# Kernel tuning notes

Measured on AMD Instinct MI355X. Metric: run time of the kernel, lower is better.

Reference implementation:

```python
import jax, jax.numpy as jnp
import numpy as np

B = 1024      # molecules in batch
M = 128       # atoms per molecule
K = 32        # max_num_neighbors
CUTOFF = 5.0  # radius cutoff


def setup_inputs() -> dict:
    key = jax.random.key(0)
    pos = jax.random.normal(key, (B * M, 3), dtype=jnp.float32) * 3.0
    batch = (jnp.arange(B * M, dtype=jnp.int32) // M).astype(jnp.int32)
    return {"pos": pos, "batch": batch}


def reference(pos, batch):
    # pos: [N,3]; batch is sorted with M atoms per molecule -> reshape [B,M,3]
    p = pos.reshape(B, M, 3)
    sq = jnp.sum(p * p, axis=-1)  # [B,M]
    # per-molecule pairwise squared distances, [B,M,M]
    d2 = sq[:, :, None] + sq[:, None, :] - 2.0 * jnp.einsum('bic,bjc->bij', p, p)
    d2 = jnp.maximum(d2, 0.0)
    valid = d2 < CUTOFF * CUTOFF  # loop=True: self (d2=0) is included
    d2m = jnp.where(valid, d2, jnp.inf)
    neg, idx = jax.lax.top_k(-d2m, K)       # K nearest in-radius, idx: [B,M,K]
    taken = jnp.isfinite(neg)                # which slots are real edges
    local_i = jnp.arange(M, dtype=idx.dtype)
    idx = jnp.where(taken, idx, local_i[None, :, None])  # pad with self index

    # gather neighbor positions: [B,M,K,3]
    p_nb = p[jnp.arange(B)[:, None, None], idx]
    vec = p_nb - p[:, :, None, :]            # pos[edge0] - pos[edge1] (source - target)

    nonself = idx != local_i[None, :, None]
    mask = taken & nonself                   # self-loops & padding get weight 0
    sqv = jnp.sum(vec * vec, axis=-1)
    weight = jnp.where(mask, jnp.sqrt(jnp.where(mask, sqv, 1.0)), 0.0)

    node_base = (jnp.arange(B, dtype=jnp.int32) * M)[:, None, None]
    src = (node_base + idx.astype(jnp.int32)).reshape(-1)                 # edge_index[0] = neighbor j
    dst = jnp.broadcast_to(node_base + local_i.astype(jnp.int32)[None, :, None], (B, M, K)).reshape(-1)
    edge_index = jnp.stack([src, dst], axis=0)          # [2, B*M*K]
    edge_weight = weight.reshape(-1)                    # [B*M*K]
    edge_vec = vec.reshape(-1, 3)                       # [B*M*K, 3]
    return edge_index, edge_weight, edge_vec
```

## Files before the change

kernel.cpp:

```cpp
#include <hip/hip_runtime.h>
#include <stdint.h>

#define BB 1024
#define MM 128
#define KK 32
#define NEDGE (BB * MM * KK)
#define BPB 4
#define ROWS_PER_WAVE (MM / (4 * BPB))

#define TH 0x41C80000u
#define INFK 0x7F800000u

typedef unsigned int uint2v __attribute__((ext_vector_type(2)));

#define DPP1 "quad_perm:[1,0,3,2] row_mask:0xf bank_mask:0xf"
#define DPP2 "quad_perm:[2,3,0,1] row_mask:0xf bank_mask:0xf"

template<int ST>
static __device__ __forceinline__ void cexd(unsigned& k, unsigned long long msk) {
    unsigned t0, t1;
    if constexpr (ST == 1) {
        asm("s_nop 1\n\t"
            "v_min_u32_dpp %1, %0, %0 " DPP1 "\n\t"
            "v_max_u32_dpp %2, %0, %0 " DPP1 "\n\t"
            "v_cndmask_b32 %0, %2, %1, %3"
            : "+v"(k), "=&v"(t0), "=&v"(t1) : "s"(msk));
    } else {
        asm("s_nop 1\n\t"
            "v_min_u32_dpp %1, %0, %0 " DPP2 "\n\t"
            "v_max_u32_dpp %2, %0, %0 " DPP2 "\n\t"
            "v_cndmask_b32 %0, %2, %1, %3"
            : "+v"(k), "=&v"(t0), "=&v"(t1) : "s"(msk));
    }
}

template<int ST>
static __device__ __forceinline__ void cexs(unsigned& k, unsigned long long msk) {
    unsigned p = (unsigned)__builtin_amdgcn_ds_swizzle((int)k, (ST << 10) | 0x1F);
    unsigned mn = __builtin_elementwise_min(k, p);
    unsigned mx = __builtin_elementwise_max(k, p);
    asm("v_cndmask_b32 %0, %1, %2, %3" : "=v"(k) : "v"(mx), "v"(mn), "s"(msk));
}

static __device__ __forceinline__ void cex32f(unsigned& k, unsigned long long msk) {
#if __has_builtin(__builtin_amdgcn_permlane32_swap)
    uint2v s = __builtin_amdgcn_permlane32_swap(k, k, false, false);
    unsigned mn = __builtin_elementwise_min(s.x, s.y);
    unsigned mx = __builtin_elementwise_max(s.x, s.y);
#else
    unsigned p = (unsigned)__shfl_xor((int)k, 32, 64);
    unsigned mn = __builtin_elementwise_min(k, p);
    unsigned mx = __builtin_elementwise_max(k, p);
#endif
    asm("v_cndmask_b32 %0, %1, %2, %3" : "=v"(k) : "v"(mx), "v"(mn), "s"(msk));
}

static __device__ __forceinline__ unsigned minxor32(unsigned k) {
#if __has_builtin(__builtin_amdgcn_permlane32_swap)
    uint2v s = __builtin_amdgcn_permlane32_swap(k, k, false, false);
    return __builtin_elementwise_min(s.x, s.y);
#else
    unsigned p = (unsigned)__shfl_xor((int)k, 32, 64);
    return __builtin_elementwise_min(k, p);
#endif
}

static __device__ __forceinline__ unsigned mbcnt64(unsigned long long m) {
    unsigned t = __builtin_amdgcn_mbcnt_lo((unsigned)m, 0u);
    return __builtin_amdgcn_mbcnt_hi((unsigned)(m >> 32), t);
}

__global__ __launch_bounds__(256, 4) void knn_edges_kernel(const float* __restrict__ pos,
                                                           float* __restrict__ out) {
    __shared__ float px[MM], py[MM], pz[MM], sqs[MM];
    __shared__ unsigned comp[4][64];
    const int blk = blockIdx.x;
    const int b = blk >> 2;
    const int sub = blk & (BPB - 1);
    const int tid = threadIdx.x;

    if (tid < MM) {
        const float* p = pos + (size_t)(b * MM + tid) * 3;
        float x = p[0], y = p[1], z = p[2];
        px[tid] = x; py[tid] = y; pz[tid] = z;
        sqs[tid] = __fadd_rn(__fadd_rn(__fmul_rn(x, x), __fmul_rn(y, y)), __fmul_rn(z, z));
    }
    __syncthreads();

    const int wave = tid >> 6;
    const int lane = tid & 63;
    const int g = lane & 31;
    const bool hi = lane >= 32;
    const unsigned upper = hi ? ~0u : 0u;

    unsigned long long m1  = 0x5555555555555555ull;
    unsigned long long m2  = 0x3333333333333333ull;
    unsigned long long m4  = 0x0F0F0F0F0F0F0F0Full;
    unsigned long long m8  = 0x00FF00FF00FF00FFull;
    unsigned long long m16 = 0x0000FFFF0000FFFFull;
    unsigned long long m32 = 0x00000000FFFFFFFFull;
    asm("" : "+s"(m1), "+s"(m2), "+s"(m4), "+s"(m8), "+s"(m16), "+s"(m32));

    auto dmask = [&](int s) -> unsigned {
        unsigned zer = ((g & s) == 0) ? ~0u : 0u;
        return ~(zer ^ upper);
    };
    const unsigned f2    = dmask(2);
    const unsigned nf2   = ~f2;
    const unsigned f4c   = dmask(4);
    const unsigned f8c   = dmask(8);
    const unsigned f16c  = dmask(16);
    const unsigned f32c  = dmask(32);
    const unsigned t24   = f2 ^ f4c;
    const unsigned t48   = f4c ^ f8c;
    const unsigned t816  = f8c ^ f16c;
    const unsigned t1632 = f16c ^ f32c;
    const unsigned nf32  = ~f32c;

    auto ff = [&](int s) -> unsigned { return (lane & s) ? ~0u : 0u; };
    const unsigned u2    = ff(2);
    const unsigned s24   = u2 ^ ff(4);
    const unsigned s48   = ff(4) ^ ff(8);
    const unsigned s816  = ff(8) ^ ff(16);
    const unsigned s1632 = ff(16) ^ ff(32);
    const unsigned u32   = ff(32);

    const int j0 = lane, j1 = lane + 64;
    const float xa = px[j0], ya = py[j0], za = pz[j0], qa = sqs[j0];
    const float xb = px[j1], yb = py[j1], zb = pz[j1], qb = sqs[j1];

    const int row0 = sub * (MM / BPB) + wave * ROWS_PER_WAVE;
    const float fbase = (float)(b * MM);

    float* const vecbase = out + 3 * (size_t)NEDGE;
    const long e0 = (long)(b * MM + row0) * KK + g;
    float* pA = hi ? out + (size_t)NEDGE + e0 : out + e0;
    float* pB = vecbase + e0 * 3 + (hi ? 2 : 0);
    float* pC = hi ? out + 2 * (size_t)NEDGE + e0 : vecbase + e0 * 3 + 1;
    const int sC = hi ? KK : 3 * KK;

    float fnode = (float)(b * MM + row0);

    for (int i = row0; i < row0 + ROWS_PER_WAVE; ++i) {
        const float xi = px[i], yi = py[i], zi = pz[i], qi = sqs[i];

        float dot0 = fmaf(xi, xa, fmaf(yi, ya, zi * za));
        float d20 = fmaxf(fmaf(-2.0f, dot0, qi + qa), 0.0f);
        unsigned k0r = (__float_as_uint(d20) & 0xFFFFFF80u) | (unsigned)j0;
        float dot1 = fmaf(xi, xb, fmaf(yi, yb, zi * zb));
        float d21 = fmaxf(fmaf(-2.0f, dot1, qi + qb), 0.0f);
        unsigned k1r = (__float_as_uint(d21) & 0xFFFFFF80u) | (unsigned)j1;

        unsigned long long mask0 = __ballot(k0r < TH);
        unsigned long long mask1 = __ballot(k1r < TH);
        unsigned c0 = (unsigned)__popcll(mask0);
        unsigned nsurv = c0 + (unsigned)__popcll(mask1);

        unsigned mdup;
        if (nsurv <= 64u) {
            unsigned dest0 = mbcnt64(mask0);
            unsigned dest1 = c0 + mbcnt64(mask1);
            if (k0r < TH) comp[wave][dest0] = k0r;
            if (k1r < TH) comp[wave][dest1] = k1r;
            asm volatile("s_waitcnt lgkmcnt(0)" ::: "memory");
            unsigned k = comp[wave][lane];
            k = ((unsigned)lane < nsurv) ? k : INFK;

            k ^= u2;
            cexd<1>(k, m1);
            k ^= s24;
            cexd<2>(k, m2); cexd<1>(k, m1);
            k ^= s48;
            cexs<4>(k, m4); cexd<2>(k, m2); cexd<1>(k, m1);
            k ^= s816;
            cexs<8>(k, m8); cexs<4>(k, m4); cexd<2>(k, m2); cexd<1>(k, m1);
            k ^= s1632;
            cexs<16>(k, m16); cexs<8>(k, m8); cexs<4>(k, m4);
            cexd<2>(k, m2); cexd<1>(k, m1);
            k ^= u32;
            cex32f(k, m32); cexs<16>(k, m16); cexs<8>(k, m8); cexs<4>(k, m4);
            cexd<2>(k, m2); cexd<1>(k, m1);

#if __has_builtin(__builtin_amdgcn_permlane32_swap)
            uint2v s = __builtin_amdgcn_permlane32_swap(k, k, false, false);
            unsigned partner = s.x ^ s.y ^ k;
#else
            unsigned partner = (unsigned)__shfl_xor((int)k, 32, 64);
#endif
            asm("v_cndmask_b32 %0, %1, %2, %3" : "=v"(mdup) : "v"(partner), "v"(k), "s"(m32));
        } else {
            unsigned K0 = k0r ^ f2;
            unsigned K1 = k1r ^ nf2;
#define SS2(ST, MSK) cexs<ST>(K0, MSK); cexs<ST>(K1, MSK);
            SS2(1, m1)
            K0 ^= t24; K1 ^= t24;
            SS2(2, m2) SS2(1, m1)
            K0 ^= t48; K1 ^= t48;
            SS2(4, m4) SS2(2, m2) SS2(1, m1)
            K0 ^= t816; K1 ^= t816;
            SS2(8, m8) SS2(4, m4) SS2(2, m2) SS2(1, m1)
            K0 ^= t1632; K1 ^= t1632;
            SS2(16, m16) SS2(8, m8) SS2(4, m4) SS2(2, m2) SS2(1, m1)
#undef SS2
            unsigned Ca = (__builtin_elementwise_min(K0 ^ f32c, K1 ^ nf32)) ^ upper;
            cexs<16>(Ca, m16); cexs<8>(Ca, m8); cexs<4>(Ca, m4);
            cexs<2>(Ca, m2);  cexs<1>(Ca, m1);
            unsigned Ma = minxor32(Ca ^ upper);
            cexs<16>(Ma, m16); cexs<8>(Ma, m8); cexs<4>(Ma, m4);
            cexs<2>(Ma, m2);  cexs<1>(Ma, m1);
            mdup = Ma;
        }

        const bool taken = mdup < TH;
        const int j = (int)(mdup & 127u);
        const int sel = taken ? j : i;

        float dxv = __fsub_rn(px[sel], xi);
        float dyv = __fsub_rn(py[sel], yi);
        float dzv = __fsub_rn(pz[sel], zi);
        float w = sqrtf(fmaf(dzv, dzv, fmaf(dyv, dyv, dxv * dxv)));
        const float fsrc = fbase + (float)sel;

        pA[0] = hi ? fnode : fsrc;
        pB[0] = hi ? dzv : dxv;
        pC[0] = hi ? w : dyv;
        pA += KK; pB += 3 * KK; pC += sC;
        fnode += 1.0f;
    }
}

extern "C" void kernel_launch(void* const* d_in, const int* in_sizes, int n_in,
                              void* d_out, int out_size, void* d_ws, size_t ws_size,
                              hipStream_t stream) {
    const float* pos = (const float*)d_in[0];
    float* out = (float*)d_out;
    hipLaunchKernelGGL(knn_edges_kernel, dim3(BB * BPB), dim3(256), 0, stream, pos, out);
}
```

Before: 39.68 us.

## Add tighter second radius filter and process one molecule per block

When more than 64 atoms fall inside the cutoff, the kernel retries compaction with a smaller threshold (d2 < 12.5). If that leaves between 32 and 64 candidates, it uses the cheap single-register bitonic sort instead of the full 128-element sort. It also drops the four-blocks-per-molecule split: one block now handles a whole molecule with 32 rows per wave, which cuts redundant position loads but reduces grid parallelism to 1024 blocks. The extra ballot adds a little cost on dense rows.

```diff
diff --git a/kernel.cpp b/kernel.cpp
--- a/kernel.cpp
+++ b/kernel.cpp
@@ -5,10 +5,10 @@
 #define MM 128
 #define KK 32
 #define NEDGE (BB * MM * KK)
-#define BPB 4
-#define ROWS_PER_WAVE (MM / (4 * BPB))
-
-#define TH 0x41C80000u
+#define ROWS_PER_WAVE 32
+
+#define TH  0x41C80000u
+#define T2  0x41480000u
 #define INFK 0x7F800000u
 
 typedef unsigned int uint2v __attribute__((ext_vector_type(2)));
@@ -65,6 +65,18 @@
 #endif
 }
 
+static __device__ __forceinline__ unsigned duphalf(unsigned k, unsigned long long m32) {
+#if __has_builtin(__builtin_amdgcn_permlane32_swap)
+    uint2v s = __builtin_amdgcn_permlane32_swap(k, k, false, false);
+    unsigned partner = s.x ^ s.y ^ k;
+#else
+    unsigned partner = (unsigned)__shfl_xor((int)k, 32, 64);
+#endif
+    unsigned r;
+    asm("v_cndmask_b32 %0, %1, %2, %3" : "=v"(r) : "v"(partner), "v"(k), "s"(m32));
+    return r;
+}
+
 static __device__ __forceinline__ unsigned mbcnt64(unsigned long long m) {
     unsigned t = __builtin_amdgcn_mbcnt_lo((unsigned)m, 0u);
     return __builtin_amdgcn_mbcnt_hi((unsigned)(m >> 32), t);
@@ -74,9 +86,7 @@
                                                            float* __restrict__ out) {
     __shared__ float px[MM], py[MM], pz[MM], sqs[MM];
     __shared__ unsigned comp[4][64];
-    const int blk = blockIdx.x;
-    const int b = blk >> 2;
-    const int sub = blk & (BPB - 1);
+    const int b = blockIdx.x;
     const int tid = threadIdx.x;
 
     if (tid < MM) {
@@ -100,6 +110,14 @@
     unsigned long long m16 = 0x0000FFFF0000FFFFull;
     unsigned long long m32 = 0x00000000FFFFFFFFull;
     asm("" : "+s"(m1), "+s"(m2), "+s"(m4), "+s"(m8), "+s"(m16), "+s"(m32));
+
+    auto ff = [&](int s) -> unsigned { return (lane & s) ? ~0u : 0u; };
+    const unsigned u2    = ff(2);
+    const unsigned s24   = u2 ^ ff(4);
+    const unsigned s48   = ff(4) ^ ff(8);
+    const unsigned s816  = ff(8) ^ ff(16);
+    const unsigned s1632 = ff(16) ^ ff(32);
+    const unsigned u32   = ff(32);
 
     auto dmask = [&](int s) -> unsigned {
         unsigned zer = ((g & s) == 0) ? ~0u : 0u;
@@ -117,19 +135,34 @@
     const unsigned t1632 = f16c ^ f32c;
     const unsigned nf32  = ~f32c;
 
-    auto ff = [&](int s) -> unsigned { return (lane & s) ? ~0u : 0u; };
-    const unsigned u2    = ff(2);
-    const unsigned s24   = u2 ^ ff(4);
-    const unsigned s48   = ff(4) ^ ff(8);
-    const unsigned s816  = ff(8) ^ ff(16);
-    const unsigned s1632 = ff(16) ^ ff(32);
-    const unsigned u32   = ff(32);
+    auto slow_sort = [&](unsigned k0r, unsigned k1r) -> unsigned {
+        unsigned K0 = k0r ^ f2;
+        unsigned K1 = k1r ^ nf2;
+#define SS2(ST, MSK) cexs<ST>(K0, MSK); cexs<ST>(K1, MSK);
+        SS2(1, m1)
+        K0 ^= t24; K1 ^= t24;
+        SS2(2, m2) SS2(1, m1)
+        K0 ^= t48; K1 ^= t48;
+        SS2(4, m4) SS2(2, m2) SS2(1, m1)
+        K0 ^= t816; K1 ^= t816;
+        SS2(8, m8) SS2(4, m4) SS2(2, m2) SS2(1, m1)
+        K0 ^= t1632; K1 ^= t1632;
+        SS2(16, m16) SS2(8, m8) SS2(4, m4) SS2(2, m2) SS2(1, m1)
+#undef SS2
+        unsigned Ca = (__builtin_elementwise_min(K0 ^ f32c, K1 ^ nf32)) ^ upper;
+        cexs<16>(Ca, m16); cexs<8>(Ca, m8); cexs<4>(Ca, m4);
+        cexs<2>(Ca, m2);  cexs<1>(Ca, m1);
+        unsigned Ma = minxor32(Ca ^ upper);
+        cexs<16>(Ma, m16); cexs<8>(Ma, m8); cexs<4>(Ma, m4);
+        cexs<2>(Ma, m2);  cexs<1>(Ma, m1);
+        return Ma;
+    };
 
     const int j0 = lane, j1 = lane + 64;
     const float xa = px[j0], ya = py[j0], za = pz[j0], qa = sqs[j0];
     const float xb = px[j1], yb = py[j1], zb = pz[j1], qb = sqs[j1];
 
-    const int row0 = sub * (MM / BPB) + wave * ROWS_PER_WAVE;
+    const int row0 = wave * ROWS_PER_WAVE;
     const float fbase = (float)(b * MM);
 
     float* const vecbase = out + 3 * (size_t)NEDGE;
@@ -139,32 +172,39 @@
     float* pC = hi ? out + 2 * (size_t)NEDGE + e0 : vecbase + e0 * 3 + 1;
     const int sC = hi ? KK : 3 * KK;
 
-    float fnode = (float)(b * MM + row0);
-
-    for (int i = row0; i < row0 + ROWS_PER_WAVE; ++i) {
+    float fnode = fbase + (float)row0;
+
+#pragma unroll 1
+    for (int ii = 0; ii < ROWS_PER_WAVE; ++ii) {
+        const int i = row0 + ii;
         const float xi = px[i], yi = py[i], zi = pz[i], qi = sqs[i];
 
         float dot0 = fmaf(xi, xa, fmaf(yi, ya, zi * za));
-        float d20 = fmaxf(fmaf(-2.0f, dot0, qi + qa), 0.0f);
-        unsigned k0r = (__float_as_uint(d20) & 0xFFFFFF80u) | (unsigned)j0;
+        unsigned k0r = (__float_as_uint(fmaxf(fmaf(-2.0f, dot0, qi + qa), 0.0f)) & 0xFFFFFF80u) | (unsigned)j0;
         float dot1 = fmaf(xi, xb, fmaf(yi, yb, zi * zb));
-        float d21 = fmaxf(fmaf(-2.0f, dot1, qi + qb), 0.0f);
-        unsigned k1r = (__float_as_uint(d21) & 0xFFFFFF80u) | (unsigned)j1;
+        unsigned k1r = (__float_as_uint(fmaxf(fmaf(-2.0f, dot1, qi + qb), 0.0f)) & 0xFFFFFF80u) | (unsigned)j1;
 
         unsigned long long mask0 = __ballot(k0r < TH);
         unsigned long long mask1 = __ballot(k1r < TH);
         unsigned c0 = (unsigned)__popcll(mask0);
-        unsigned nsurv = c0 + (unsigned)__popcll(mask1);
+        unsigned n  = c0 + (unsigned)__popcll(mask1);
+
+        bool sortable = (n <= 64u);
+        if (!sortable) {
+            mask0 = __ballot(k0r < T2);
+            mask1 = __ballot(k1r < T2);
+            c0 = (unsigned)__popcll(mask0);
+            n  = c0 + (unsigned)__popcll(mask1);
+            sortable = (n >= 32u && n <= 64u);
+        }
 
         unsigned mdup;
-        if (nsurv <= 64u) {
-            unsigned dest0 = mbcnt64(mask0);
-            unsigned dest1 = c0 + mbcnt64(mask1);
-            if (k0r < TH) comp[wave][dest0] = k0r;
-            if (k1r < TH) comp[wave][dest1] = k1r;
+        if (sortable) {
+            if ((mask0 >> lane) & 1ull) comp[wave][mbcnt64(mask0)] = k0r;
+            if ((mask1 >> lane) & 1ull) comp[wave][c0 + mbcnt64(mask1)] = k1r;
             asm volatile("s_waitcnt lgkmcnt(0)" ::: "memory");
             unsigned k = comp[wave][lane];
-            k = ((unsigned)lane < nsurv) ? k : INFK;
+            k = ((unsigned)lane < n) ? k : INFK;
 
             k ^= u2;
             cexd<1>(k, m1);
@@ -181,34 +221,9 @@
             cex32f(k, m32); cexs<16>(k, m16); cexs<8>(k, m8); cexs<4>(k, m4);
             cexd<2>(k, m2); cexd<1>(k, m1);
 
-#if __has_builtin(__builtin_amdgcn_permlane32_swap)
-            uint2v s = __builtin_amdgcn_permlane32_swap(k, k, false, false);
-            unsigned partner = s.x ^ s.y ^ k;
-#else
-            unsigned partner = (unsigned)__shfl_xor((int)k, 32, 64);
-#endif
-            asm("v_cndmask_b32 %0, %1, %2, %3" : "=v"(mdup) : "v"(partner), "v"(k), "s"(m32));
+            mdup = duphalf(k, m32);
         } else {
-            unsigned K0 = k0r ^ f2;
-            unsigned K1 = k1r ^ nf2;
-#define SS2(ST, MSK) cexs<ST>(K0, MSK); cexs<ST>(K1, MSK);
-            SS2(1, m1)
-            K0 ^= t24; K1 ^= t24;
-            SS2(2, m2) SS2(1, m1)
-            K0 ^= t48; K1 ^= t48;
-            SS2(4, m4) SS2(2, m2) SS2(1, m1)
-            K0 ^= t816; K1 ^= t816;
-            SS2(8, m8) SS2(4, m4) SS2(2, m2) SS2(1, m1)
-            K0 ^= t1632; K1 ^= t1632;
-            SS2(16, m16) SS2(8, m8) SS2(4, m4) SS2(2, m2) SS2(1, m1)
-#undef SS2
-            unsigned Ca = (__builtin_elementwise_min(K0 ^ f32c, K1 ^ nf32)) ^ upper;
-            cexs<16>(Ca, m16); cexs<8>(Ca, m8); cexs<4>(Ca, m4);
-            cexs<2>(Ca, m2);  cexs<1>(Ca, m1);
-            unsigned Ma = minxor32(Ca ^ upper);
-            cexs<16>(Ma, m16); cexs<8>(Ma, m8); cexs<4>(Ma, m4);
-            cexs<2>(Ma, m2);  cexs<1>(Ma, m1);
-            mdup = Ma;
+            mdup = slow_sort(k0r, k1r);
         }
 
         const bool taken = mdup < TH;
@@ -234,5 +249,5 @@
                               hipStream_t stream) {
     const float* pos = (const float*)d_in[0];
     float* out = (float*)d_out;
-    hipLaunchKernelGGL(knn_edges_kernel, dim3(BB * BPB), dim3(256), 0, stream, pos, out);
-}
+    hipLaunchKernelGGL(knn_edges_kernel, dim3(BB), dim3(256), 0, stream, pos, out);
+}
```

New measurement: 46.64 us. 17.5% more time.
